# Kernel optimization log

Hardware: AMD Instinct MI355X
Metric: run time of the kernel (lower is better)

The kernel has to match this reference:

```python
import jax, jax.numpy as jnp
import numpy as np

PH, PW = 7, 7      # pool_shape
SCALE = 1.0        # spatial_scale of PrRoIPool2D


def _tent_int(t):
    """Antiderivative of the bilinear tent kernel max(0, 1-|t|), clipped.
    Integral of tent from -inf to t."""
    t = jnp.clip(t, -1.0, 1.0)
    return jnp.where(t < 0.0, 0.5 * (t + 1.0) ** 2, 1.0 - 0.5 * (1.0 - t) ** 2)


def _axis_weights(lo, hi, n_bins, size):
    """Exact per-pixel integration weights along one axis.
    lo, hi: [R] roi edges. Returns (w [R, n_bins, size], bin_size [R]).
    w[r,k,i] = integral over bin k of tent(x - i) dx, so that
    sum_i F[i] * w[r,k,i] is the exact integral of the linearly
    interpolated signal F over bin k (Precise RoI Pooling)."""
    binsz = (hi - lo) / n_bins                       # [R]
    k = jnp.arange(n_bins, dtype=lo.dtype)
    a = lo[:, None] + k[None, :] * binsz[:, None]    # [R, n_bins] bin starts
    b = a + binsz[:, None]                           # bin ends
    i = jnp.arange(size, dtype=lo.dtype)             # pixel coordinates
    w = _tent_int(b[:, :, None] - i[None, None, :]) - _tent_int(a[:, :, None] - i[None, None, :])
    return w, binsz


def setup_inputs() -> dict:
    key = jax.random.key(0)
    k1, k2, k3, k4, k5 = jax.random.split(key, 5)
    B, C, H, W = 8, 64, 64, 64
    N = 512  # rois per leading dim; total R = N * B = 4096
    feature = jax.random.normal(k1, (B, C, H, W), dtype=jnp.float32)
    bidx = jax.random.randint(k2, (N, B, 1, 1), 0, B).astype(jnp.float32)
    x1 = jax.random.uniform(k3, (N, B, 1, 1), minval=0.0, maxval=W - 12.0)
    y1 = jax.random.uniform(k4, (N, B, 1, 1), minval=0.0, maxval=H - 12.0)
    wh = jax.random.uniform(k5, (N, B, 1, 1, 2), minval=4.0, maxval=12.0)
    x2 = x1 + wh[..., 0]
    y2 = y1 + wh[..., 1]
    rois = jnp.stack([bidx, x1, y1, x2, y2], axis=-1)  # [N, B, 1, 1, 5]
    return {"feature": feature, "rois": rois}


def reference(feature, rois):
    B, C, H, W = feature.shape
    # rois.permute([1,0,2,3,4]).reshape(-1, 5)
    r = jnp.transpose(rois, (1, 0, 2, 3, 4)).reshape(-1, 5)  # [R, 5]
    bidx = r[:, 0].astype(jnp.int32)
    x1 = r[:, 1] * SCALE
    y1 = r[:, 2] * SCALE
    x2 = r[:, 3] * SCALE
    y2 = r[:, 4] * SCALE

    wx, bw = _axis_weights(x1, x2, PW, W)  # [R, PW, W], [R]
    wy, bh = _axis_weights(y1, y2, PH, H)  # [R, PH, H], [R]

    # Route each ROI to its feature-batch entry without materializing
    # a [R, C, H, W] gather: fold the batch one-hot into the y-weights.
    onehot = (bidx[:, None] == jnp.arange(B)[None, :]).astype(feature.dtype)  # [R, B]
    wy_b = wy[:, :, None, :] * onehot[:, None, :, None]                      # [R, PH, B, H]

    tmp = jnp.einsum('rubi,bcij->rucj', wy_b, feature)  # [R, PH, C, W]
    integ = jnp.einsum('rucj,rvj->rcuv', tmp, wx)       # [R, C, PH, PW]

    area = jnp.maximum(bw * bh, 0.0)[:, None, None, None]
    bins = jnp.where(area > 0, integ / jnp.maximum(area, 1e-12), 0.0)

    # AvgPool2d(pool_shape) over the full (PH, PW) grid -> [R, C, 1, 1]
    out = jnp.mean(bins, axis=(2, 3), keepdims=True)
    return out
```

## Files before the change

### kernel.cpp

```cpp
#include <hip/hip_runtime.h>

constexpr int B = 8, C = 64, H = 64, W = 64;
constexpr int N = 512;
constexpr int R = N * B;
constexpr int HW = H * W;

__device__ __forceinline__ float tent_int(float t) {
    t = fminf(1.0f, fmaxf(-1.0f, t));
    float u = t + 1.0f;
    float v = 1.0f - t;
    return (t < 0.0f) ? 0.5f * u * u : 1.0f - 0.5f * v * v;
}

__device__ __forceinline__ float bf_lo(unsigned int u) {
    union { unsigned int i; float f; } c; c.i = u << 16; return c.f;
}
__device__ __forceinline__ float bf_hi(unsigned int u) {
    union { unsigned int i; float f; } c; c.i = u & 0xFFFF0000u; return c.f;
}
__device__ __forceinline__ unsigned short f2bf(float x) {
    union { float f; unsigned int i; } c; c.f = x;
    unsigned int r = c.i + 0x7FFFu + ((c.i >> 16) & 1u);
    return (unsigned short)(r >> 16);
}

__global__ __launch_bounds__(256) void transpose_kernel(
    const float* __restrict__ in,
    unsigned short* __restrict__ out)
{
    __shared__ float tile[64][65];
    const int b  = blockIdx.x >> 6;
    const int tp = (blockIdx.x & 63) * 64;
    const int t  = threadIdx.x;
    const int tq = t >> 6;
    const int tl = t & 63;

    const float* src = in + (size_t)b * C * HW;
    #pragma unroll
    for (int s = 0; s < 16; ++s) {
        int c = s * 4 + tq;
        tile[c][tl] = src[(size_t)c * HW + tp + tl];
    }
    __syncthreads();
    unsigned short* dst = out + ((size_t)b * HW + tp) * C;
    #pragma unroll
    for (int s = 0; s < 16; ++s) {
        int p = s * 4 + tq;
        dst[(size_t)p * C + tl] = f2bf(tile[tl][p]);
    }
}

__global__ __launch_bounds__(256) void prroi_main(
    const unsigned short* __restrict__ ft,
    const float* __restrict__ rois,
    float* __restrict__ out)
{
    const int r    = blockIdx.x;
    const int wid  = threadIdx.x >> 6;
    const int lane = threadIdx.x & 63;
    const int pg   = lane >> 3;
    const int cg   = lane & 7;

    const int bo = r >> 9;
    const int n  = r & 511;
    const float* rp = rois + ((size_t)n * B + bo) * 5;

    const int   b  = (int)rp[0];
    const float x1 = rp[1], y1 = rp[2], x2 = rp[3], y2 = rp[4];

    const int i_lo = max(0, (int)ceilf(y1 - 1.0f));
    const int i_hi = min(H - 1, (int)floorf(y2 + 1.0f));
    const int j_lo = max(0, (int)ceilf(x1 - 1.0f));
    const int j_hi = min(W - 1, (int)floorf(x2 + 1.0f));
    const int ny = i_hi - i_lo + 1;
    const int nx = j_hi - j_lo + 1;
    const int nk = (nx + 7) >> 3;

    float wx[2];
    int   coff[2];
    #pragma unroll
    for (int k = 0; k < 2; ++k) {
        const int  jj    = k * 8 + pg;
        const int  j     = j_lo + jj;
        const bool valid = (jj < nx);
        const float jf   = (float)j;
        wx[k]   = valid ? (tent_int(x2 - jf) - tent_int(x1 - jf)) : 0.0f;
        coff[k] = min(j, W - 1) * C + cg * 8;
    }

    float acc[8] = {0.f, 0.f, 0.f, 0.f, 0.f, 0.f, 0.f, 0.f};
    const unsigned short* fb = ft + (size_t)b * HW * C;
    for (int ii = wid; ii < ny; ii += 4) {
        const int i  = i_lo + ii;
        const float fi = (float)i;
        const float wy = tent_int(y2 - fi) - tent_int(y1 - fi);
        const unsigned short* rowp = fb + (size_t)i * (W * C);
        #pragma unroll 2
        for (int k = 0; k < nk; ++k) {
            const uint4 u = *reinterpret_cast<const uint4*>(rowp + coff[k]);
            const float w = wy * wx[k];
            acc[0] = fmaf(w, bf_lo(u.x), acc[0]);
            acc[1] = fmaf(w, bf_hi(u.x), acc[1]);
            acc[2] = fmaf(w, bf_lo(u.y), acc[2]);
            acc[3] = fmaf(w, bf_hi(u.y), acc[3]);
            acc[4] = fmaf(w, bf_lo(u.z), acc[4]);
            acc[5] = fmaf(w, bf_hi(u.z), acc[5]);
            acc[6] = fmaf(w, bf_lo(u.w), acc[6]);
            acc[7] = fmaf(w, bf_hi(u.w), acc[7]);
        }
    }

    #pragma unroll
    for (int e = 0; e < 8; ++e) {
        acc[e] += __shfl_xor(acc[e], 8);
        acc[e] += __shfl_xor(acc[e], 16);
        acc[e] += __shfl_xor(acc[e], 32);
    }

    __shared__ float part[4][8][8];
    if (pg == 0) {
        #pragma unroll
        for (int e = 0; e < 8; ++e) part[wid][cg][e] = acc[e];
    }
    __syncthreads();

    if (threadIdx.x < 64) {
        const int c = threadIdx.x;
        const int g = c >> 3, e = c & 7;
        const float s = (part[0][g][e] + part[1][g][e]) +
                        (part[2][g][e] + part[3][g][e]);
        const float prod  = (x2 - x1) * (y2 - y1);
        const float scale = (prod > 0.0f) ? (1.0f / fmaxf(prod, 49e-12f)) : 0.0f;
        out[(size_t)r * C + c] = s * scale;
    }
}

__global__ __launch_bounds__(64) void prroi_fallback(
    const float* __restrict__ feature, const float* __restrict__ rois,
    float* __restrict__ out)
{
    const int r  = blockIdx.x;
    const int bo = r / N;
    const int n  = r - bo * N;
    const float* rp = rois + ((size_t)n * B + bo) * 5;
    const float x1 = rp[1], y1 = rp[2], x2 = rp[3], y2 = rp[4];
    const int b = (int)rp[0];
    int i_lo = max(0, (int)ceilf(y1 - 1.0f));
    int i_hi = min(H - 1, (int)floorf(y2 + 1.0f));
    int j_lo = max(0, (int)ceilf(x1 - 1.0f));
    int j_hi = min(W - 1, (int)floorf(x2 + 1.0f));
    const int ny = i_hi - i_lo + 1;
    const int nx = j_hi - j_lo + 1;
    __shared__ float sWy[16], sWx[16];
    const int t = threadIdx.x;
    if (t < 16) {
        int i = i_lo + t;
        sWy[t] = (t < ny) ? (tent_int(y2 - (float)i) - tent_int(y1 - (float)i)) : 0.0f;
    } else if (t < 32) {
        int tt = t - 16, j = j_lo + tt;
        sWx[tt] = (tt < nx) ? (tent_int(x2 - (float)j) - tent_int(x1 - (float)j)) : 0.0f;
    }
    __syncthreads();
    const float* fb = feature + ((size_t)b * C + t) * HW;
    float acc = 0.0f;
    for (int ii = 0; ii < ny; ++ii) {
        const float* row = fb + (size_t)(i_lo + ii) * W + j_lo;
        float rowsum = 0.0f;
        for (int jj = 0; jj < nx; ++jj) rowsum = fmaf(sWx[jj], row[jj], rowsum);
        acc = fmaf(sWy[ii], rowsum, acc);
    }
    const float bw = (x2 - x1) * (1.0f / 7.0f), bh = (y2 - y1) * (1.0f / 7.0f);
    const float area = fmaxf(bw * bh, 0.0f);
    out[(size_t)r * C + t] = (area > 0.0f) ? (acc / (49.0f * fmaxf(area, 1e-12f))) : 0.0f;
}

extern "C" void kernel_launch(void* const* d_in, const int* in_sizes, int n_in,
                              void* d_out, int out_size, void* d_ws, size_t ws_size,
                              hipStream_t stream) {
    const float* feature = (const float*)d_in[0];
    const float* rois    = (const float*)d_in[1];
    float* out           = (float*)d_out;

    const size_t need = (size_t)B * HW * C * sizeof(unsigned short);
    if (ws_size >= need) {
        unsigned short* ft = (unsigned short*)d_ws;
        transpose_kernel<<<B * (HW / 64), 256, 0, stream>>>(feature, ft);
        prroi_main<<<R, 256, 0, stream>>>(ft, rois, out);
    } else {
        prroi_fallback<<<R, 64, 0, stream>>>(feature, rois, out);
    }
}
```

Before: 71.90 us.

## Use one wavefront per ROI and drop shared-memory cross-wave reduction

The main kernel now runs each ROI with a single 64-lane wavefront that loops over every feature row, instead of four wavefronts splitting rows. This removes the shared-memory partial buffer, the __syncthreads barrier and the final cross-wave sum. Output is written with vectorized float4 stores from 8 lanes. The trade-off is less parallelism per ROI (longer serial row loop per wave), offset by a smaller block and no idle waves when ny is small.

```diff
diff --git a/kernel.cpp b/kernel.cpp
--- a/kernel.cpp
+++ b/kernel.cpp
@@ -50,13 +50,12 @@
     }
 }
 
-__global__ __launch_bounds__(256) void prroi_main(
+__global__ __launch_bounds__(64) void prroi_main(
     const unsigned short* __restrict__ ft,
     const float* __restrict__ rois,
     float* __restrict__ out)
 {
     const int r    = blockIdx.x;
-    const int wid  = threadIdx.x >> 6;
     const int lane = threadIdx.x & 63;
     const int pg   = lane >> 3;
     const int cg   = lane & 7;
@@ -89,12 +88,11 @@
     }
 
     float acc[8] = {0.f, 0.f, 0.f, 0.f, 0.f, 0.f, 0.f, 0.f};
-    const unsigned short* fb = ft + (size_t)b * HW * C;
-    for (int ii = wid; ii < ny; ii += 4) {
-        const int i  = i_lo + ii;
-        const float fi = (float)i;
+    const unsigned short* fb = ft + ((size_t)b * HW + (size_t)i_lo * W) * C;
+    for (int ii = 0; ii < ny; ++ii) {
+        const float fi = (float)(i_lo + ii);
         const float wy = tent_int(y2 - fi) - tent_int(y1 - fi);
-        const unsigned short* rowp = fb + (size_t)i * (W * C);
+        const unsigned short* rowp = fb + (size_t)ii * (W * C);
         #pragma unroll 2
         for (int k = 0; k < nk; ++k) {
             const uint4 u = *reinterpret_cast<const uint4*>(rowp + coff[k]);
@@ -117,21 +115,17 @@
         acc[e] += __shfl_xor(acc[e], 32);
     }
 
-    __shared__ float part[4][8][8];
-    if (pg == 0) {
-        #pragma unroll
-        for (int e = 0; e < 8; ++e) part[wid][cg][e] = acc[e];
-    }
-    __syncthreads();
+    const float prod  = (x2 - x1) * (y2 - y1);
+    const float scale = (prod > 0.0f) ? (1.0f / fmaxf(prod, 49e-12f)) : 0.0f;
 
-    if (threadIdx.x < 64) {
-        const int c = threadIdx.x;
-        const int g = c >> 3, e = c & 7;
-        const float s = (part[0][g][e] + part[1][g][e]) +
-                        (part[2][g][e] + part[3][g][e]);
-        const float prod  = (x2 - x1) * (y2 - y1);
-        const float scale = (prod > 0.0f) ? (1.0f / fmaxf(prod, 49e-12f)) : 0.0f;
-        out[(size_t)r * C + c] = s * scale;
+    if (lane < 8) {
+        float* op = out + (size_t)r * C + lane * 8;
+        float4 lo = make_float4(acc[0] * scale, acc[1] * scale,
+                                acc[2] * scale, acc[3] * scale);
+        float4 hi = make_float4(acc[4] * scale, acc[5] * scale,
+                                acc[6] * scale, acc[7] * scale);
+        *reinterpret_cast<float4*>(op)     = lo;
+        *reinterpret_cast<float4*>(op + 4) = hi;
     }
 }
 
@@ -185,7 +179,7 @@
     if (ws_size >= need) {
         unsigned short* ft = (unsigned short*)d_ws;
         transpose_kernel<<<B * (HW / 64), 256, 0, stream>>>(feature, ft);
-        prroi_main<<<R, 256, 0, stream>>>(ft, rois, out);
+        prroi_main<<<R, 64, 0, stream>>>(ft, rois, out);
     } else {
         prroi_fallback<<<R, 64, 0, stream>>>(feature, rois, out);
     }
```

Result: no change. 71.53 us, median of 2 (-0.5%).
